# Kernel tuning notes

Hardware: AMD Instinct MI355X
Metric: run time of the kernel (lower is better)

## Reference

```python
import jax, jax.numpy as jnp
import numpy as np

# Mamba2 defaults (mamba_ssm)
D_MODEL = 512
EXPAND = 2
D_INNER = EXPAND * D_MODEL          # 1024
D_STATE = 128
HEADDIM = 64
NHEADS = D_INNER // HEADDIM         # 16
NGROUPS = 1
D_CONV = 4
CONV_DIM = D_INNER + 2 * NGROUPS * D_STATE   # 1280
D_IN_PROJ = 2 * D_INNER + 2 * NGROUPS * D_STATE + NHEADS  # 2320
N_LAYERS = 2
EPS = 1e-5


def silu(x):
    return x * jax.nn.sigmoid(x)


def mamba2_layer(x, in_w, conv_w, conv_b, dt_bias, A_log, D_skip, norm_w, out_w):
    b, l, _ = x.shape
    zxbcdt = x @ in_w                                   # (b,l,2320)
    z = zxbcdt[..., :D_INNER]                           # (b,l,1024)
    xBC = zxbcdt[..., D_INNER:D_INNER + CONV_DIM]       # (b,l,1280)
    dt = zxbcdt[..., D_INNER + CONV_DIM:]               # (b,l,16)

    # causal depthwise conv1d, kernel D_CONV
    xBC_pad = jnp.pad(xBC, ((0, 0), (D_CONV - 1, 0), (0, 0)))
    xBC = sum(xBC_pad[:, k:k + l, :] * conv_w[k] for k in range(D_CONV)) + conv_b
    xBC = silu(xBC)

    xh = xBC[..., :D_INNER].reshape(b, l, NHEADS, HEADDIM)     # (b,l,h,p)
    B = xBC[..., D_INNER:D_INNER + D_STATE]                    # (b,l,n)
    C = xBC[..., D_INNER + D_STATE:]                           # (b,l,n)

    dt = jax.nn.softplus(dt + dt_bias)                         # (b,l,h)
    dA = jnp.exp(dt * (-jnp.exp(A_log)))                       # (b,l,h)

    def step(h, inp):
        dA_t, dt_t, B_t, C_t, x_t = inp
        # h: (b,h,p,n)
        h = dA_t[:, :, None, None] * h + jnp.einsum('bh,bhp,bn->bhpn', dt_t, x_t, B_t)
        y_t = jnp.einsum('bhpn,bn->bhp', h, C_t)
        return h, y_t

    h0 = jnp.zeros((b, NHEADS, HEADDIM, D_STATE), x.dtype)
    xs = (dA.transpose(1, 0, 2), dt.transpose(1, 0, 2),
          B.transpose(1, 0, 2), C.transpose(1, 0, 2),
          xh.transpose(1, 0, 2, 3))
    _, ys = jax.lax.scan(step, h0, xs)                         # (l,b,h,p)
    y = ys.transpose(1, 0, 2, 3) + D_skip[None, None, :, None] * xh
    y = y.reshape(b, l, D_INNER)

    # gated RMSNorm: norm(y * silu(z)) * weight
    y = y * silu(z)
    y = y * jax.lax.rsqrt(jnp.mean(y * y, axis=-1, keepdims=True) + EPS) * norm_w
    return y @ out_w


def setup_inputs() -> dict:
    key = jax.random.key(0)
    ks = jax.random.split(key, 10)
    L = N_LAYERS
    x = jax.random.normal(ks[0], (4, 2048, D_MODEL), dtype=jnp.float32)
    s_in = 1.0 / np.sqrt(D_MODEL)
    s_out = 1.0 / np.sqrt(D_INNER)
    in_w = jax.random.normal(ks[1], (L, D_MODEL, D_IN_PROJ), jnp.float32) * s_in
    conv_w = jax.random.normal(ks[2], (L, D_CONV, CONV_DIM), jnp.float32) * (1.0 / np.sqrt(D_CONV))
    conv_b = jnp.zeros((L, 1, 1, CONV_DIM), jnp.float32)[:, 0, 0, :]
    dt_bias = jnp.log(jnp.expm1(jax.random.uniform(ks[3], (L, NHEADS), jnp.float32, 1e-3, 0.1)))
    A_log = jnp.log(jax.random.uniform(ks[4], (L, NHEADS), jnp.float32, 1.0, 16.0))
    D_skip = jnp.ones((L, NHEADS), jnp.float32)
    norm_w = jnp.ones((L, D_INNER), jnp.float32)
    out_w = jax.random.normal(ks[5], (L, D_INNER, D_MODEL), jnp.float32) * s_out
    return {"x": x, "in_w": in_w, "conv_w": conv_w, "conv_b": conv_b,
            "dt_bias": dt_bias, "A_log": A_log, "D_skip": D_skip,
            "norm_w": norm_w, "out_w": out_w}


def reference(x, in_w, conv_w, conv_b, dt_bias, A_log, D_skip, norm_w, out_w):
    for i in range(N_LAYERS):
        x = mamba2_layer(x, in_w[i], conv_w[i], conv_b[i], dt_bias[i],
                         A_log[i], D_skip[i], norm_w[i], out_w[i])
    return x
```

## Files before the change

### kernel.cpp

```cpp
#include <hip/hip_runtime.h>
#include <hip/hip_bf16.h>
#include <cstddef>
#include <cstdint>


#define BATCH 4
#define SEQ   2048
#define DMODEL 512
#define DINNER 1024
#define DSTATE 128
#define HEADDIM 64
#define NHEADS 16
#define DCONV 4
#define CONVDIM 1280
#define DINPROJ 2320
#define NPAD_IN 2432
#define ROWS (BATCH * SEQ)
#define NSEG 32
#define TSEG 64

#define SWZ32(r, c)  ((r) * 32  + (((((c) >> 3) ^ (((r) >> 1) & 3)) << 3) | ((c) & 7)))
#define SWZ64(r, c)  ((r) * 64  + (((((c) >> 3) ^ ((r) & 7)) << 3) | ((c) & 7)))
#define SWZ128(r, c) ((r) * 128 + (((((c) >> 3) ^ ((r) & 7)) << 3) | ((c) & 7)))

typedef __attribute__((ext_vector_type(8))) short bf16x8;
typedef __attribute__((ext_vector_type(4))) float f32x4;

__device__ __forceinline__ float silu_f(float x) {
    return x * (1.0f / (1.0f + __expf(-x)));
}
__device__ __forceinline__ unsigned short f2bfu(float f) {
    unsigned u = __float_as_uint(f);
    unsigned r = u + 0x7FFFu + ((u >> 16) & 1u);
    return (unsigned short)(r >> 16);
}
__device__ __forceinline__ float bfu2f(unsigned short h) {
    return __uint_as_float(((unsigned)h) << 16);
}

__global__ __launch_bounds__(256)
void split_a_kernel(const float* __restrict__ A,
                    unsigned short* __restrict__ Ah,
                    unsigned short* __restrict__ Al)
{
    const size_t i = ((size_t)blockIdx.x * 256 + threadIdx.x) * 8;
    const float4 a = *(const float4*)&A[i];
    const float4 b = *(const float4*)&A[i + 4];
    float v[8] = {a.x, a.y, a.z, a.w, b.x, b.y, b.z, b.w};
    unsigned hv[8], lv[8];
#pragma unroll
    for (int j = 0; j < 8; ++j) {
        hv[j] = f2bfu(v[j]);
        lv[j] = f2bfu(v[j] - bfu2f((unsigned short)hv[j]));
    }
    uint4 ph = make_uint4(hv[0] | (hv[1] << 16), hv[2] | (hv[3] << 16),
                          hv[4] | (hv[5] << 16), hv[6] | (hv[7] << 16));
    uint4 pl = make_uint4(lv[0] | (lv[1] << 16), lv[2] | (lv[3] << 16),
                          lv[4] | (lv[5] << 16), lv[6] | (lv[7] << 16));
    *(uint4*)&Ah[i] = ph;
    *(uint4*)&Al[i] = pl;
}

__global__ __launch_bounds__(256)
void tsplit_w_kernel(const float* __restrict__ W, int K, int N,
                     unsigned short* __restrict__ Oh,
                     unsigned short* __restrict__ Ol)
{
    __shared__ float tile[32][33];
    const int n0 = blockIdx.x * 32, k0 = blockIdx.y * 32;
    const int c = threadIdx.x & 31, r8 = threadIdx.x >> 5;
    const int n = n0 + c;
#pragma unroll
    for (int i = 0; i < 4; ++i) {
        const int k = r8 + i * 8;
        float v = 0.0f;
        if (n < N) v = W[(size_t)(k0 + k) * N + n];
        tile[c][k] = v;
    }
    __syncthreads();
#pragma unroll
    for (int i = 0; i < 4; ++i) {
        const int nl = r8 + i * 8;
        const float v = tile[nl][c];
        const unsigned short h = f2bfu(v);
        const unsigned short l = f2bfu(v - bfu2f(h));
        const size_t o = (size_t)(n0 + nl) * K + k0 + c;
        Oh[o] = h;
        Ol[o] = l;
    }
}

__global__ __launch_bounds__(256)
void tsplit_chunk_kernel(const float* __restrict__ src, int K, int N, int rs,
                         size_t chunkStride,
                         unsigned short* __restrict__ Oh,
                         unsigned short* __restrict__ Ol)
{
    __shared__ float tile[32][33];
    const int z = blockIdx.z;
    const float* W = src + (size_t)z * chunkStride;
    const int n0 = blockIdx.x * 32, k0 = blockIdx.y * 32;
    const int c = threadIdx.x & 31, r8 = threadIdx.x >> 5;
#pragma unroll
    for (int i = 0; i < 4; ++i) {
        const int k = r8 + i * 8;
        tile[c][k] = W[(size_t)(k0 + k) * rs + n0 + c];
    }
    __syncthreads();
#pragma unroll
    for (int i = 0; i < 4; ++i) {
        const int nl = r8 + i * 8;
        const float v = tile[nl][c];
        const unsigned short h = f2bfu(v);
        const unsigned short l = f2bfu(v - bfu2f(h));
        const size_t o = (size_t)z * N * K + (size_t)(n0 + nl) * K + k0 + c;
        Oh[o] = h;
        Ol[o] = l;
    }
}

__global__ __launch_bounds__(256)
void gemm_bf16s(const unsigned short* __restrict__ Ah,
                const unsigned short* __restrict__ Al,
                const unsigned short* __restrict__ Bh,
                const unsigned short* __restrict__ Bl,
                float* __restrict__ C, int ldc, int N, int K,
                int exactCol0)
{
    __shared__ __align__(16) unsigned short As[2][128 * 32];
    __shared__ __align__(16) unsigned short Bs[2][128 * 32];

    const int tid = threadIdx.x;
    const int w = tid >> 6, lane = tid & 63;
    const int wm = w >> 1, wn = w & 1;

    const int nwg = gridDim.x * gridDim.y;
    int flat = blockIdx.y * gridDim.x + blockIdx.x;
    flat = (flat & 7) * (nwg >> 3) + (flat >> 3);
    const int bx = flat % gridDim.x, by = flat / gridDim.x;
    const int row0 = by * 128, col0 = bx * 128;
    const bool exact = (col0 + 128 > exactCol0);

    const int srow = tid >> 1;
    const int sk   = (tid & 1) * 16;

    const int lr = lane & 15;
    const int lk = (lane >> 4) * 8;

    f32x4 acc[4][4];
#pragma unroll
    for (int i = 0; i < 4; ++i)
#pragma unroll
        for (int j = 0; j < 4; ++j) acc[i][j] = (f32x4){0.f, 0.f, 0.f, 0.f};

    const int sw0 = SWZ32(srow, sk);
    const int sw1 = SWZ32(srow, sk + 8);
    const size_t gabase = (size_t)(row0 + srow) * K + sk;
    const size_t gbbase = (size_t)(col0 + srow) * K + sk;

    uint4 vah0 = *(const uint4*)&Ah[gabase];
    uint4 vah1 = *(const uint4*)&Ah[gabase + 8];
    uint4 val0 = *(const uint4*)&Al[gabase];
    uint4 val1 = *(const uint4*)&Al[gabase + 8];
    uint4 vbh0 = *(const uint4*)&Bh[gbbase];
    uint4 vbh1 = *(const uint4*)&Bh[gbbase + 8];

    for (int k0 = 0; k0 < K; k0 += 32) {
        __syncthreads();
        *(uint4*)&As[0][sw0] = vah0;  *(uint4*)&As[0][sw1] = vah1;
        *(uint4*)&As[1][sw0] = val0;  *(uint4*)&As[1][sw1] = val1;
        *(uint4*)&Bs[0][sw0] = vbh0;  *(uint4*)&Bs[0][sw1] = vbh1;
        if (exact) {
            const size_t gb = gbbase + k0;
            *(uint4*)&Bs[1][sw0] = *(const uint4*)&Bl[gb];
            *(uint4*)&Bs[1][sw1] = *(const uint4*)&Bl[gb + 8];
        }
        __syncthreads();

        if (k0 + 32 < K) {
            const size_t ga = gabase + k0 + 32;
            const size_t gb = gbbase + k0 + 32;
            vah0 = *(const uint4*)&Ah[ga];
            vah1 = *(const uint4*)&Ah[ga + 8];
            val0 = *(const uint4*)&Al[ga];
            val1 = *(const uint4*)&Al[ga + 8];
            vbh0 = *(const uint4*)&Bh[gb];
            vbh1 = *(const uint4*)&Bh[gb + 8];
        }

        bf16x8 a_h[4], a_l[4], b_h[4];
#pragma unroll
        for (int mt = 0; mt < 4; ++mt) {
            const int r = wm * 64 + mt * 16 + lr;
            a_h[mt] = *(const bf16x8*)&As[0][SWZ32(r, lk)];
            a_l[mt] = *(const bf16x8*)&As[1][SWZ32(r, lk)];
        }
#pragma unroll
        for (int nt = 0; nt < 4; ++nt) {
            const int c = wn * 64 + nt * 16 + lr;
            b_h[nt] = *(const bf16x8*)&Bs[0][SWZ32(c, lk)];
        }
#pragma unroll
        for (int mt = 0; mt < 4; ++mt)
#pragma unroll
            for (int nt = 0; nt < 4; ++nt) {
                acc[mt][nt] = __builtin_amdgcn_mfma_f32_16x16x32_bf16(a_h[mt], b_h[nt], acc[mt][nt], 0, 0, 0);
                acc[mt][nt] = __builtin_amdgcn_mfma_f32_16x16x32_bf16(a_l[mt], b_h[nt], acc[mt][nt], 0, 0, 0);
            }
        if (exact) {
            bf16x8 b_l[4];
#pragma unroll
            for (int nt = 0; nt < 4; ++nt) {
                const int c = wn * 64 + nt * 16 + lr;
                b_l[nt] = *(const bf16x8*)&Bs[1][SWZ32(c, lk)];
            }
#pragma unroll
            for (int mt = 0; mt < 4; ++mt)
#pragma unroll
                for (int nt = 0; nt < 4; ++nt)
                    acc[mt][nt] = __builtin_amdgcn_mfma_f32_16x16x32_bf16(a_h[mt], b_l[nt], acc[mt][nt], 0, 0, 0);
        }
    }

    const int crow = (lane >> 4) * 4;
#pragma unroll
    for (int mt = 0; mt < 4; ++mt)
#pragma unroll
        for (int nt = 0; nt < 4; ++nt) {
            const int cc = col0 + wn * 64 + nt * 16 + lr;
            if (cc < N) {
#pragma unroll
                for (int r = 0; r < 4; ++r)
                    C[(size_t)(row0 + wm * 64 + mt * 16 + crow + r) * ldc + cc] = acc[mt][nt][r];
            }
        }
}

__global__ __launch_bounds__(320)
void conv_kernel(const float* __restrict__ zx,
                 const float* __restrict__ cw,
                 const float* __restrict__ cb,
                 const float* __restrict__ dtbias,
                 const float* __restrict__ alog,
                 float* __restrict__ xh,
                 float* __restrict__ Bb,
                 float* __restrict__ Cb,
                 unsigned short* __restrict__ Bsph,
                 unsigned short* __restrict__ Bspl,
                 unsigned short* __restrict__ Csph,
                 unsigned short* __restrict__ Cspl,
                 float* __restrict__ dtb,
                 float* __restrict__ dAb)
{
    const int row = blockIdx.x;
    const int l   = row & (SEQ - 1);
    const int c4  = threadIdx.x * 4;

    float4 acc = *(const float4*)&cb[c4];
#pragma unroll
    for (int k = 0; k < DCONV; ++k) {
        const int lk = l - (DCONV - 1) + k;
        if (lk >= 0) {
            const float4 v = *(const float4*)&zx[(size_t)(row - (DCONV - 1) + k) * DINPROJ + DINNER + c4];
            const float4 w = *(const float4*)&cw[k * CONVDIM + c4];
            acc.x = fmaf(v.x, w.x, acc.x);
            acc.y = fmaf(v.y, w.y, acc.y);
            acc.z = fmaf(v.z, w.z, acc.z);
            acc.w = fmaf(v.w, w.w, acc.w);
        }
    }
    acc.x = silu_f(acc.x);
    acc.y = silu_f(acc.y);
    acc.z = silu_f(acc.z);
    acc.w = silu_f(acc.w);

    if (c4 < DINNER) {
        *(float4*)&xh[(size_t)row * DINNER + c4] = acc;
    } else {
        float o[4] = {acc.x, acc.y, acc.z, acc.w};
        unsigned hv[4], lv[4];
#pragma unroll
        for (int j = 0; j < 4; ++j) {
            hv[j] = f2bfu(o[j]);
            lv[j] = f2bfu(o[j] - bfu2f((unsigned short)hv[j]));
        }
        const uint2 ph = make_uint2(hv[0] | (hv[1] << 16), hv[2] | (hv[3] << 16));
        const uint2 pl = make_uint2(lv[0] | (lv[1] << 16), lv[2] | (lv[3] << 16));
        if (c4 < DINNER + DSTATE) {
            const size_t oi = (size_t)row * DSTATE + (c4 - DINNER);
            *(float4*)&Bb[oi] = acc;
            *(uint2*)&Bsph[oi] = ph;
            *(uint2*)&Bspl[oi] = pl;
        } else {
            const size_t oi = (size_t)row * DSTATE + (c4 - DINNER - DSTATE);
            *(float4*)&Cb[oi] = acc;
            *(uint2*)&Csph[oi] = ph;
            *(uint2*)&Cspl[oi] = pl;
        }
    }

    if (threadIdx.x < NHEADS) {
        const int hh = threadIdx.x;
        const float raw = zx[(size_t)row * DINPROJ + (DINNER + CONVDIM) + hh] + dtbias[hh];
        const float dtv = (raw > 20.0f) ? raw : log1pf(expf(raw));
        const float a = expf(alog[hh]);
        dtb[row * NHEADS + hh] = dtv;
        dAb[row * NHEADS + hh] = expf(-a * dtv);
    }
}

__global__ __launch_bounds__(64)
void meta_kernel(const float* __restrict__ dtb,
                 const float* __restrict__ alog,
                 float* __restrict__ lB, float* __restrict__ wB,
                 float* __restrict__ ptot)
{
    const int bhc = blockIdx.x;
    const int chunk = bhc & 31;
    const int h = (bhc >> 5) & 15;
    const int b = bhc >> 9;
    const int t = threadIdx.x;
    const size_t row0 = (size_t)b * SEQ + (size_t)chunk * TSEG;

    const float a = __expf(alog[h]);
    const float dtv = dtb[(row0 + t) * NHEADS + h];
    float v = -a * dtv;
#pragma unroll
    for (int off = 1; off < 64; off <<= 1) {
        const float u = __shfl_up(v, off, 64);
        if (t >= off) v += u;
    }
    const float l63 = __shfl(v, 63, 64);
    lB[(size_t)bhc * 64 + t] = v;
    wB[(size_t)bhc * 64 + t] = __expf(l63 - v) * dtv;
    if (t == 0) ptot[bhc] = __expf(l63);
}

__global__ __launch_bounds__(256)
void cb_kernel(const unsigned short* __restrict__ Ch,
               const unsigned short* __restrict__ Cl,
               const unsigned short* __restrict__ Bh_,
               const unsigned short* __restrict__ Bl_,
               float* __restrict__ CBo)
{
    __shared__ __align__(16) unsigned short Cs[2][64 * 128];
    __shared__ __align__(16) unsigned short Bs2[2][64 * 128];
    const int bc = blockIdx.x;
    const size_t base = (size_t)bc * 8192;
    const int tid = threadIdx.x;
#pragma unroll
    for (int i = 0; i < 4; ++i) {
        const int bi = tid + i * 256;
        const int r = bi >> 4, c = (bi & 15) << 3;
        const int d = SWZ128(r, c);
        *(uint4*)&Cs[0][d]  = ((const uint4*)(Ch  + base))[bi];
        *(uint4*)&Cs[1][d]  = ((const uint4*)(Cl  + base))[bi];
        *(uint4*)&Bs2[0][d] = ((const uint4*)(Bh_ + base))[bi];
        *(uint4*)&Bs2[1][d] = ((const uint4*)(Bl_ + base))[bi];
    }
    __syncthreads();

    const int w = tid >> 6, lane = tid & 63;
    const int lr = lane & 15, lk = (lane >> 4) * 8;
    f32x4 acc[4];
#pragma unroll
    for (int i = 0; i < 4; ++i) acc[i] = (f32x4){0.f, 0.f, 0.f, 0.f};

#pragma unroll
    for (int kk = 0; kk < 4; ++kk) {
        const int k0 = kk * 32;
        const int ar = w * 16 + lr;
        const bf16x8 ah = *(const bf16x8*)&Cs[0][SWZ128(ar, k0 + lk)];
        const bf16x8 al = *(const bf16x8*)&Cs[1][SWZ128(ar, k0 + lk)];
#pragma unroll
        for (int st = 0; st < 4; ++st) {
            const int br = st * 16 + lr;
            const bf16x8 bh = *(const bf16x8*)&Bs2[0][SWZ128(br, k0 + lk)];
            const bf16x8 bl = *(const bf16x8*)&Bs2[1][SWZ128(br, k0 + lk)];
            acc[st] = __builtin_amdgcn_mfma_f32_16x16x32_bf16(ah, bh, acc[st], 0, 0, 0);
            acc[st] = __builtin_amdgcn_mfma_f32_16x16x32_bf16(ah, bl, acc[st], 0, 0, 0);
            acc[st] = __builtin_amdgcn_mfma_f32_16x16x32_bf16(al, bh, acc[st], 0, 0, 0);
        }
    }
    const int crow = (lane >> 4) * 4;
#pragma unroll
    for (int st = 0; st < 4; ++st)
#pragma unroll
        for (int r = 0; r < 4; ++r)
            CBo[(size_t)bc * 4096 + (size_t)(w * 16 + crow + r) * 64 + st * 16 + lr] = acc[st][r];
}

__global__ __launch_bounds__(256)
void state_kernel(const unsigned short* __restrict__ BTh,
                  const unsigned short* __restrict__ BTl,
                  const float* __restrict__ xh,
                  const float* __restrict__ wB,
                  unsigned short* __restrict__ hloc)
{
    __shared__ __align__(16) unsigned short BTs[2][128 * 64];
    __shared__ __align__(16) unsigned short xwT[2][64 * 64];

    const int bhc = blockIdx.x;
    const int chunk = bhc & 31;
    const int h = (bhc >> 5) & 15;
    const int b = bhc >> 9;
    const int bc = b * 32 + chunk;
    const size_t row0 = (size_t)b * SEQ + (size_t)chunk * TSEG;
    const int tid = threadIdx.x;

    const size_t bbase = (size_t)bc * 8192;
#pragma unroll
    for (int i = 0; i < 4; ++i) {
        const int bi = tid + i * 256;
        const int r = bi >> 3, c = (bi & 7) << 3;
        const int d = SWZ64(r, c);
        *(uint4*)&BTs[0][d] = ((const uint4*)(BTh + bbase))[bi];
        *(uint4*)&BTs[1][d] = ((const uint4*)(BTl + bbase))[bi];
    }
    {
        const int t = tid & 63;
        const int pb = (tid >> 6) * 16;
        const float wv = wB[(size_t)bhc * 64 + t];
        const float* xr = &xh[(row0 + t) * DINNER + h * HEADDIM + pb];
#pragma unroll
        for (int i = 0; i < 16; ++i) {
            const int p = pb + i;
            const float v = xr[i] * wv;
            const unsigned short hh = f2bfu(v);
            const int d = SWZ64(p, t);
            xwT[0][d] = hh;
            xwT[1][d] = f2bfu(v - bfu2f(hh));
        }
    }
    __syncthreads();

    const int w = tid >> 6, lane = tid & 63;
    const int lr = lane & 15, lk = (lane >> 4) * 8;
    f32x4 acc[2][4];
#pragma unroll
    for (int i = 0; i < 2; ++i)
#pragma unroll
        for (int j = 0; j < 4; ++j) acc[i][j] = (f32x4){0.f, 0.f, 0.f, 0.f};

#pragma unroll
    for (int kk = 0; kk < 2; ++kk) {
        const int k0 = kk * 32;
        bf16x8 ah[2], al[2];
#pragma unroll
        for (int nt = 0; nt < 2; ++nt) {
            const int n = w * 32 + nt * 16 + lr;
            ah[nt] = *(const bf16x8*)&BTs[0][SWZ64(n, k0 + lk)];
            al[nt] = *(const bf16x8*)&BTs[1][SWZ64(n, k0 + lk)];
        }
#pragma unroll
        for (int pt = 0; pt < 4; ++pt) {
            const int pr = pt * 16 + lr;
            const bf16x8 bh = *(const bf16x8*)&xwT[0][SWZ64(pr, k0 + lk)];
            const bf16x8 bl = *(const bf16x8*)&xwT[1][SWZ64(pr, k0 + lk)];
#pragma unroll
            for (int nt = 0; nt < 2; ++nt) {
                acc[nt][pt] = __builtin_amdgcn_mfma_f32_16x16x32_bf16(ah[nt], bh, acc[nt][pt], 0, 0, 0);
                acc[nt][pt] = __builtin_amdgcn_mfma_f32_16x16x32_bf16(ah[nt], bl, acc[nt][pt], 0, 0, 0);
                acc[nt][pt] = __builtin_amdgcn_mfma_f32_16x16x32_bf16(al[nt], bh, acc[nt][pt], 0, 0, 0);
            }
        }
    }

    const int crow = (lane >> 4) * 4;
#pragma unroll
    for (int nt = 0; nt < 2; ++nt)
#pragma unroll
        for (int pt = 0; pt < 4; ++pt)
#pragma unroll
            for (int r = 0; r < 4; ++r) {
                const int n = w * 32 + nt * 16 + crow + r;
                hloc[(size_t)bhc * 8192 + (size_t)n * 64 + pt * 16 + lr] = f2bfu(acc[nt][pt][r]);
            }
}

__global__ __launch_bounds__(256)
void combine_kernel(unsigned short* __restrict__ hloc,
                    const float* __restrict__ ptot)
{
    const int bid = blockIdx.x;
    const int bh = bid >> 3;
    const int chunk = bid & 7;
    const int e0 = chunk * 1024 + threadIdx.x * 4;

    float s0 = 0.f, s1 = 0.f, s2 = 0.f, s3 = 0.f;
    for (int k = 0; k < NSEG; ++k) {
        unsigned short* p = &hloc[((size_t)bh * NSEG + k) * 8192 + e0];
        const uint2 vp = *(const uint2*)p;
        const float v0 = bfu2f((unsigned short)(vp.x & 0xffff));
        const float v1 = bfu2f((unsigned short)(vp.x >> 16));
        const float v2 = bfu2f((unsigned short)(vp.y & 0xffff));
        const float v3 = bfu2f((unsigned short)(vp.y >> 16));
        uint2 op;
        op.x = (unsigned)f2bfu(s0) | ((unsigned)f2bfu(s1) << 16);
        op.y = (unsigned)f2bfu(s2) | ((unsigned)f2bfu(s3) << 16);
        *(uint2*)p = op;
        const float pt = ptot[bh * NSEG + k];
        s0 = fmaf(pt, s0, v0);
        s1 = fmaf(pt, s1, v1);
        s2 = fmaf(pt, s2, v2);
        s3 = fmaf(pt, s3, v3);
    }
}

__global__ __launch_bounds__(512)
void y_kernel(const unsigned short* __restrict__ Ch,
              const float* __restrict__ CBg,
              const float* __restrict__ lB,
              const float* __restrict__ dtb,
              const float* __restrict__ xh,
              const unsigned short* __restrict__ hloc,
              float* __restrict__ yb)
{
    __shared__ __align__(16) unsigned short CsA[64 * 128];
    __shared__ __align__(16) unsigned short opB[64 * 128];
    __shared__ __align__(16) unsigned short Ms[64 * 64];
    __shared__ float ls4[256], dt4[256];

    const int gid = blockIdx.x;
    const int hg = gid & 3, bc = gid >> 2;
    const int chunk = bc & 31, b = bc >> 5;
    const size_t row0 = (size_t)b * SEQ + (size_t)chunk * TSEG;
    const int tid = threadIdx.x;

    const size_t cbase = (size_t)bc * 8192;
#pragma unroll
    for (int i = 0; i < 2; ++i) {
        const int bi = tid + i * 512;
        const int r = bi >> 4, c = (bi & 15) << 3;
        *(uint4*)&CsA[SWZ128(r, c)] = ((const uint4*)(Ch + cbase))[bi];
    }
    if (tid < 256) {
        const int e = tid >> 6, t = tid & 63;
        const int h = hg * 4 + e;
        const int bhc = (b * NHEADS + h) * NSEG + chunk;
        ls4[tid] = lB[(size_t)bhc * 64 + t];
        dt4[tid] = dtb[(row0 + t) * NHEADS + h];
    }
    __syncthreads();

    const int w = tid >> 6, lane = tid & 63;
    const int lr = lane & 15, lk = (lane >> 4) * 8;
    const int tt = w & 3, ph = w >> 2;
    const int crow = (lane >> 4) * 4;
    const float* CBc = CBg + (size_t)bc * 4096;

    for (int e = 0; e < 4; ++e) {
        const int h = hg * 4 + e;
        const int bhc = (b * NHEADS + h) * NSEG + chunk;
        const unsigned short* h0p = hloc + (size_t)bhc * 8192;

        {
            const int n = tid & 127;
            const int pb = (tid >> 7) * 16;
            const unsigned short* hr = &h0p[(size_t)n * 64 + pb];
#pragma unroll
            for (int i = 0; i < 16; ++i)
                opB[SWZ128(pb + i, n)] = hr[i];
        }
        __syncthreads();

        f32x4 acc[2];
        acc[0] = (f32x4){0.f, 0.f, 0.f, 0.f};
        acc[1] = (f32x4){0.f, 0.f, 0.f, 0.f};
#pragma unroll
        for (int kk = 0; kk < 4; ++kk) {
            const int k0 = kk * 32;
            const bf16x8 ah = *(const bf16x8*)&CsA[SWZ128(tt * 16 + lr, k0 + lk)];
#pragma unroll
            for (int pt = 0; pt < 2; ++pt) {
                const int pc = (ph * 2 + pt) * 16 + lr;
                const bf16x8 bh = *(const bf16x8*)&opB[SWZ128(pc, k0 + lk)];
                acc[pt] = __builtin_amdgcn_mfma_f32_16x16x32_bf16(ah, bh, acc[pt], 0, 0, 0);
            }
        }
        {
            float el[4];
#pragma unroll
            for (int r = 0; r < 4; ++r) el[r] = __expf(ls4[e * 64 + tt * 16 + crow + r]);
#pragma unroll
            for (int pt = 0; pt < 2; ++pt)
#pragma unroll
                for (int r = 0; r < 4; ++r) acc[pt][r] *= el[r];
        }
        __syncthreads();

#pragma unroll
        for (int i = 0; i < 8; ++i) {
            const int lin = tid * 8 + i;
            const int t = lin >> 6, s = lin & 63;
            float m = 0.0f;
            if (s <= t)
                m = CBc[t * 64 + s] * dt4[e * 64 + s] * __expf(ls4[e * 64 + t] - ls4[e * 64 + s]);
            Ms[SWZ64(t, s)] = f2bfu(m);
        }
        {
            const int s = tid & 63;
            const int pb = (tid >> 6) * 8;
            const float* xr = &xh[(row0 + s) * DINNER + h * HEADDIM + pb];
#pragma unroll
            for (int i = 0; i < 8; ++i) {
                const int p = pb + i;
                opB[SWZ64(p, s)] = f2bfu(xr[i]);
            }
        }
        __syncthreads();

#pragma unroll
        for (int kk = 0; kk < 2; ++kk) {
            const int k0 = kk * 32;
            const bf16x8 ah = *(const bf16x8*)&Ms[SWZ64(tt * 16 + lr, k0 + lk)];
#pragma unroll
            for (int pt = 0; pt < 2; ++pt) {
                const int pc = (ph * 2 + pt) * 16 + lr;
                const bf16x8 bh = *(const bf16x8*)&opB[SWZ64(pc, k0 + lk)];
                acc[pt] = __builtin_amdgcn_mfma_f32_16x16x32_bf16(ah, bh, acc[pt], 0, 0, 0);
            }
        }

#pragma unroll
        for (int pt = 0; pt < 2; ++pt)
#pragma unroll
            for (int r = 0; r < 4; ++r)
                yb[(row0 + tt * 16 + crow + r) * DINNER + h * HEADDIM + (ph * 2 + pt) * 16 + lr] = acc[pt][r];
        __syncthreads();
    }
}

__global__ __launch_bounds__(256)
void gate_kernel(const float* __restrict__ yb,
                 const float* __restrict__ xh,
                 const float* __restrict__ dskip,
                 const float* __restrict__ zx,
                 const float* __restrict__ nw,
                 unsigned short* __restrict__ yh,
                 unsigned short* __restrict__ yl)
{
    const int row = blockIdx.x;
    const int c4 = threadIdx.x * 4;

    float4 y = *(const float4*)&yb[(size_t)row * DINNER + c4];
    const float4 xv = *(const float4*)&xh[(size_t)row * DINNER + c4];
    const float dsk = dskip[c4 >> 6];
    y.x = fmaf(dsk, xv.x, y.x);
    y.y = fmaf(dsk, xv.y, y.y);
    y.z = fmaf(dsk, xv.z, y.z);
    y.w = fmaf(dsk, xv.w, y.w);

    const float4 z = *(const float4*)&zx[(size_t)row * DINPROJ + c4];
    float4 g;
    g.x = y.x * silu_f(z.x);
    g.y = y.y * silu_f(z.y);
    g.z = y.z * silu_f(z.z);
    g.w = y.w * silu_f(z.w);

    float local = g.x * g.x + g.y * g.y + g.z * g.z + g.w * g.w;
#pragma unroll
    for (int m = 32; m >= 1; m >>= 1) local += __shfl_xor(local, m, 64);

    __shared__ float red[4];
    if ((threadIdx.x & 63) == 0) red[threadIdx.x >> 6] = local;
    __syncthreads();
    const float total = red[0] + red[1] + red[2] + red[3];
    const float scale = rsqrtf(total * (1.0f / (float)DINNER) + 1e-5f);

    const float4 w = *(const float4*)&nw[c4];
    float o[4];
    o[0] = g.x * scale * w.x;
    o[1] = g.y * scale * w.y;
    o[2] = g.z * scale * w.z;
    o[3] = g.w * scale * w.w;

    unsigned hv[4], lv[4];
#pragma unroll
    for (int j = 0; j < 4; ++j) {
        hv[j] = f2bfu(o[j]);
        lv[j] = f2bfu(o[j] - bfu2f((unsigned short)hv[j]));
    }
    const size_t oi = (size_t)row * DINNER + c4;
    *(uint2*)&yh[oi] = make_uint2(hv[0] | (hv[1] << 16), hv[2] | (hv[3] << 16));
    *(uint2*)&yl[oi] = make_uint2(lv[0] | (lv[1] << 16), lv[2] | (lv[3] << 16));
}

extern "C" void kernel_launch(void* const* d_in, const int* in_sizes, int n_in,
                              void* d_out, int out_size, void* d_ws, size_t ws_size,
                              hipStream_t stream)
{
    const float* x_in    = (const float*)d_in[0];
    const float* in_w    = (const float*)d_in[1];
    const float* conv_w  = (const float*)d_in[2];
    const float* conv_b  = (const float*)d_in[3];
    const float* dt_bias = (const float*)d_in[4];
    const float* A_log   = (const float*)d_in[5];
    const float* D_skip  = (const float*)d_in[6];
    const float* norm_w  = (const float*)d_in[7];
    const float* out_w   = (const float*)d_in[8];
    float* out = (float*)d_out;

    float* ws   = (float*)d_ws;
    float* zx   = ws;
    float* xh   = zx   + (size_t)ROWS * DINPROJ;
    float* Bb   = xh   + (size_t)ROWS * DINNER;
    float* Cb   = Bb   + (size_t)ROWS * DSTATE;
    float* dtb  = Cb   + (size_t)ROWS * DSTATE;
    float* dAb  = dtb  + (size_t)ROWS * NHEADS;
    float* yb   = dAb  + (size_t)ROWS * NHEADS;
    float* UN   = yb   + (size_t)ROWS * DINNER;
    float* BtF  = UN   + (size_t)16777216;
    float* WtF  = BtF  + (size_t)1245184;
    float* ptot = WtF  + (size_t)524288;
    float* lB   = ptot + (size_t)2048;
    float* wB   = lB   + (size_t)131072;
    float* BTf  = wB   + (size_t)131072;
    float* Bspf = BTf  + (size_t)1048576;
    float* Cspf = Bspf + (size_t)1048576;
    float* CBb  = Cspf + (size_t)1048576;

    unsigned short* Ah = (unsigned short*)UN;
    unsigned short* Al = Ah + (size_t)ROWS * DMODEL;
    unsigned short* hloc_us = (unsigned short*)UN;
    unsigned short* yh = (unsigned short*)UN;
    unsigned short* yl = yh + (size_t)ROWS * DINNER;

    unsigned short* Bth = (unsigned short*)BtF;
    unsigned short* Btl = Bth + (size_t)NPAD_IN * DMODEL;
    unsigned short* Wth = (unsigned short*)WtF;
    unsigned short* Wtl = Wth + (size_t)DMODEL * DINNER;

    unsigned short* BTh = (unsigned short*)BTf;
    unsigned short* BTl = BTh + (size_t)128 * 8192;
    unsigned short* Bsph = (unsigned short*)Bspf;
    unsigned short* Bspl = Bsph + (size_t)ROWS * DSTATE;
    unsigned short* Csph = (unsigned short*)Cspf;
    unsigned short* Cspl = Csph + (size_t)ROWS * DSTATE;

    for (int layer = 0; layer < 2; ++layer) {
        const float* xl = (layer == 0) ? x_in : out;

        split_a_kernel<<<(ROWS * DMODEL) / (256 * 8), 256, 0, stream>>>(xl, Ah, Al);

        tsplit_w_kernel<<<dim3(NPAD_IN / 32, DMODEL / 32), 256, 0, stream>>>(
            in_w + (size_t)layer * DMODEL * DINPROJ, DMODEL, DINPROJ, Bth, Btl);

        gemm_bf16s<<<dim3(NPAD_IN / 128, ROWS / 128), 256, 0, stream>>>(
            Ah, Al, Bth, Btl, zx, DINPROJ, DINPROJ, DMODEL,
            DINNER + CONVDIM);

        conv_kernel<<<ROWS, CONVDIM / 4, 0, stream>>>(
            zx,
            conv_w + (size_t)layer * DCONV * CONVDIM,
            conv_b + (size_t)layer * CONVDIM,
            dt_bias + (size_t)layer * NHEADS,
            A_log + (size_t)layer * NHEADS,
            xh, Bb, Cb, Bsph, Bspl, Csph, Cspl, dtb, dAb);

        meta_kernel<<<BATCH * NHEADS * NSEG, 64, 0, stream>>>(
            dtb, A_log + (size_t)layer * NHEADS, lB, wB, ptot);

        tsplit_chunk_kernel<<<dim3(128 / 32, 64 / 32, BATCH * NSEG), 256, 0, stream>>>(
            Bb, TSEG, DSTATE, DSTATE, (size_t)TSEG * DSTATE, BTh, BTl);

        cb_kernel<<<BATCH * NSEG, 256, 0, stream>>>(Csph, Cspl, Bsph, Bspl, CBb);

        state_kernel<<<BATCH * NHEADS * NSEG, 256, 0, stream>>>(
            BTh, BTl, xh, wB, hloc_us);

        combine_kernel<<<BATCH * NHEADS * 8, 256, 0, stream>>>(hloc_us, ptot);

        y_kernel<<<BATCH * NSEG * 4, 512, 0, stream>>>(
            Csph, CBb, lB, dtb, xh, hloc_us, yb);

        gate_kernel<<<ROWS, 256, 0, stream>>>(
            yb, xh, D_skip + (size_t)layer * NHEADS,
            zx, norm_w + (size_t)layer * DINNER, yh, yl);

        tsplit_w_kernel<<<dim3(DMODEL / 32, DINNER / 32), 256, 0, stream>>>(
            out_w + (size_t)layer * DINNER * DMODEL, DINNER, DMODEL, Wth, Wtl);

        gemm_bf16s<<<dim3(DMODEL / 128, ROWS / 128), 256, 0, stream>>>(
            yh, yl, Wth, Wtl, out, DMODEL, DMODEL, DINNER,
            1 << 30);
    }
}
```

Measured before the change: 467.2 us.

## Fuse D-skip into y_kernel with bf16 output and fuse A-split into out-proj GEMM

The D-skip add moves into the y_kernel epilogue, which now writes y as bf16, so gate_kernel reads half the bytes and no longer reads xh. The layer-0 output GEMM also writes the hi/lo bf16 split of its result, so the layer-1 split_a_kernel launch is dropped. Ah/Al move to a separate offset in the UN buffer so they are not overwritten by hloc/yh. The trade-off is that y is stored at bf16 precision before the gated RMSNorm, which may lose accuracy, and the GEMM epilogue does extra stores.

Measured after the change: 457.6 us. -2.1%, faster.

```diff
diff --git a/kernel.cpp b/kernel.cpp
--- a/kernel.cpp
+++ b/kernel.cpp
@@ -125,7 +125,9 @@
                 const unsigned short* __restrict__ Bh,
                 const unsigned short* __restrict__ Bl,
                 float* __restrict__ C, int ldc, int N, int K,
-                int exactCol0)
+                int exactCol0,
+                unsigned short* __restrict__ Soh,
+                unsigned short* __restrict__ Sol)
 {
     __shared__ __align__(16) unsigned short As[2][128 * 32];
     __shared__ __align__(16) unsigned short Bs[2][128 * 32];
@@ -230,8 +232,16 @@
             const int cc = col0 + wn * 64 + nt * 16 + lr;
             if (cc < N) {
 #pragma unroll
-                for (int r = 0; r < 4; ++r)
-                    C[(size_t)(row0 + wm * 64 + mt * 16 + crow + r) * ldc + cc] = acc[mt][nt][r];
+                for (int r = 0; r < 4; ++r) {
+                    const size_t oi = (size_t)(row0 + wm * 64 + mt * 16 + crow + r) * ldc + cc;
+                    const float v = acc[mt][nt][r];
+                    C[oi] = v;
+                    if (Soh) {
+                        const unsigned short h16 = f2bfu(v);
+                        Soh[oi] = h16;
+                        Sol[oi] = f2bfu(v - bfu2f(h16));
+                    }
+                }
             }
         }
 }
@@ -514,7 +524,8 @@
               const float* __restrict__ dtb,
               const float* __restrict__ xh,
               const unsigned short* __restrict__ hloc,
-              float* __restrict__ yb)
+              const float* __restrict__ dskip,
+              unsigned short* __restrict__ ybh)
 {
     __shared__ __align__(16) unsigned short CsA[64 * 128];
     __shared__ __align__(16) unsigned short opB[64 * 128];
@@ -553,6 +564,7 @@
         const int h = hg * 4 + e;
         const int bhc = (b * NHEADS + h) * NSEG + chunk;
         const unsigned short* h0p = hloc + (size_t)bhc * 8192;
+        const float dsk = dskip[h];
 
         {
             const int n = tid & 127;
@@ -625,16 +637,18 @@
 #pragma unroll
         for (int pt = 0; pt < 2; ++pt)
 #pragma unroll
-            for (int r = 0; r < 4; ++r)
-                yb[(row0 + tt * 16 + crow + r) * DINNER + h * HEADDIM + (ph * 2 + pt) * 16 + lr] = acc[pt][r];
+            for (int r = 0; r < 4; ++r) {
+                const size_t row = row0 + tt * 16 + crow + r;
+                const int col = h * HEADDIM + (ph * 2 + pt) * 16 + lr;
+                const float v = acc[pt][r] + dsk * xh[row * DINNER + col];
+                ybh[row * DINNER + col] = f2bfu(v);
+            }
         __syncthreads();
     }
 }
 
 __global__ __launch_bounds__(256)
-void gate_kernel(const float* __restrict__ yb,
-                 const float* __restrict__ xh,
-                 const float* __restrict__ dskip,
+void gate_kernel(const unsigned short* __restrict__ ybh,
                  const float* __restrict__ zx,
                  const float* __restrict__ nw,
                  unsigned short* __restrict__ yh,
@@ -643,13 +657,12 @@
     const int row = blockIdx.x;
     const int c4 = threadIdx.x * 4;
 
-    float4 y = *(const float4*)&yb[(size_t)row * DINNER + c4];
-    const float4 xv = *(const float4*)&xh[(size_t)row * DINNER + c4];
-    const float dsk = dskip[c4 >> 6];
-    y.x = fmaf(dsk, xv.x, y.x);
-    y.y = fmaf(dsk, xv.y, y.y);
-    y.z = fmaf(dsk, xv.z, y.z);
-    y.w = fmaf(dsk, xv.w, y.w);
+    const uint2 yv = *(const uint2*)&ybh[(size_t)row * DINNER + c4];
+    float4 y;
+    y.x = bfu2f((unsigned short)(yv.x & 0xffff));
+    y.y = bfu2f((unsigned short)(yv.x >> 16));
+    y.z = bfu2f((unsigned short)(yv.y & 0xffff));
+    y.w = bfu2f((unsigned short)(yv.y >> 16));
 
     const float4 z = *(const float4*)&zx[(size_t)row * DINPROJ + c4];
     float4 g;
@@ -720,11 +733,12 @@
     float* Cspf = Bspf + (size_t)1048576;
     float* CBb  = Cspf + (size_t)1048576;
 
-    unsigned short* Ah = (unsigned short*)UN;
-    unsigned short* Al = Ah + (size_t)ROWS * DMODEL;
+    unsigned short* ybh = (unsigned short*)yb;
     unsigned short* hloc_us = (unsigned short*)UN;
     unsigned short* yh = (unsigned short*)UN;
     unsigned short* yl = yh + (size_t)ROWS * DINNER;
+    unsigned short* Ah = (unsigned short*)UN + 16777216;
+    unsigned short* Al = Ah + (size_t)ROWS * DMODEL;
 
     unsigned short* Bth = (unsigned short*)BtF;
     unsigned short* Btl = Bth + (size_t)NPAD_IN * DMODEL;
@@ -739,16 +753,15 @@
     unsigned short* Cspl = Csph + (size_t)ROWS * DSTATE;
 
     for (int layer = 0; layer < 2; ++layer) {
-        const float* xl = (layer == 0) ? x_in : out;
-
-        split_a_kernel<<<(ROWS * DMODEL) / (256 * 8), 256, 0, stream>>>(xl, Ah, Al);
+        if (layer == 0)
+            split_a_kernel<<<(ROWS * DMODEL) / (256 * 8), 256, 0, stream>>>(x_in, Ah, Al);
 
         tsplit_w_kernel<<<dim3(NPAD_IN / 32, DMODEL / 32), 256, 0, stream>>>(
             in_w + (size_t)layer * DMODEL * DINPROJ, DMODEL, DINPROJ, Bth, Btl);
 
         gemm_bf16s<<<dim3(NPAD_IN / 128, ROWS / 128), 256, 0, stream>>>(
             Ah, Al, Bth, Btl, zx, DINPROJ, DINPROJ, DMODEL,
-            DINNER + CONVDIM);
+            DINNER + CONVDIM, nullptr, nullptr);
 
         conv_kernel<<<ROWS, CONVDIM / 4, 0, stream>>>(
             zx,
@@ -772,17 +785,19 @@
         combine_kernel<<<BATCH * NHEADS * 8, 256, 0, stream>>>(hloc_us, ptot);
 
         y_kernel<<<BATCH * NSEG * 4, 512, 0, stream>>>(
-            Csph, CBb, lB, dtb, xh, hloc_us, yb);
+            Csph, CBb, lB, dtb, xh, hloc_us,
+            D_skip + (size_t)layer * NHEADS, ybh);
 
         gate_kernel<<<ROWS, 256, 0, stream>>>(
-            yb, xh, D_skip + (size_t)layer * NHEADS,
-            zx, norm_w + (size_t)layer * DINNER, yh, yl);
+            ybh, zx, norm_w + (size_t)layer * DINNER, yh, yl);
 
         tsplit_w_kernel<<<dim3(DMODEL / 32, DINNER / 32), 256, 0, stream>>>(
             out_w + (size_t)layer * DINNER * DMODEL, DINNER, DMODEL, Wth, Wtl);
 
         gemm_bf16s<<<dim3(DMODEL / 128, ROWS / 128), 256, 0, stream>>>(
             yh, yl, Wth, Wtl, out, DMODEL, DMODEL, DINNER,
-            1 << 30);
-    }
-}
+            1 << 30,
+            (layer == 0) ? Ah : nullptr,
+            (layer == 0) ? Al : nullptr);
+    }
+}
```
